# Kernel tuning notes

Hardware: AMD Instinct MI355X
Metric: run time of the kernel (lower is better)

The kernel has to match this reference:

```python
import jax, jax.numpy as jnp
import numpy as np

PAD_IDX = 1  # matches init_kwargs pad_idx
TLEN, BATCH, D_IN = 50, 16, 512
SRC_LEN, VOCAB, CVOCAB = 200, 20000, 20400


def setup_inputs() -> dict:
    key = jax.random.key(0)
    k1, k2, k3, k4, k5, k6, k7 = jax.random.split(key, 7)
    hidden = jax.random.normal(k1, (TLEN, BATCH, D_IN), dtype=jnp.float32)
    attn = jax.random.uniform(k2, (TLEN, BATCH, SRC_LEN), dtype=jnp.float32)
    # src_map is a sparse one-hot indicator: each source position maps to one extended-vocab id
    src_ids = jax.random.randint(k3, (SRC_LEN, BATCH), 0, CVOCAB)
    src_map = jax.nn.one_hot(src_ids, CVOCAB, dtype=jnp.float32)  # (src_len, batch, cvocab)
    s = 1.0 / np.sqrt(D_IN)
    W = jax.random.uniform(k4, (VOCAB, D_IN), dtype=jnp.float32, minval=-s, maxval=s)
    b = jax.random.uniform(k5, (VOCAB,), dtype=jnp.float32, minval=-s, maxval=s)
    Wc = jax.random.uniform(k6, (1, D_IN), dtype=jnp.float32, minval=-s, maxval=s)
    bc = jax.random.uniform(k7, (1,), dtype=jnp.float32, minval=-s, maxval=s)
    return {"hidden": hidden, "attn": attn, "src_map": src_map, "W": W, "b": b, "Wc": Wc, "bc": bc}


def reference(hidden, attn, src_map, W, b, Wc, bc):
    tlen, batch, _ = hidden.shape
    src_len, _, cvocab = src_map.shape
    logits = jnp.einsum('tbd,vd->tbv', hidden, W) + b            # (tlen, batch, vocab)
    # faithful to torch: logits[:, pad_idx] = -inf (indexes the batch dim!)
    logits = logits.at[:, PAD_IDX, :].set(-jnp.inf)
    prob = jax.nn.softmax(logits, axis=1)                        # softmax over dim 1, as in source
    p_copy = jax.nn.sigmoid(jnp.einsum('tbd,od->tbo', hidden, Wc) + bc)  # (tlen, batch, 1)
    out_prob = prob * (1.0 - p_copy)                             # (tlen, batch, vocab)
    mul_attn = attn * p_copy                                     # (tlen, batch, src_len)
    # bmm over batch with one-hot src_map: effectively a scatter-add into extended vocab
    copy_prob = jnp.einsum('tbs,sbv->tbv', mul_attn, src_map)    # (tlen, batch, cvocab)
    # faithful to the split/stack/transpose permutation in the source
    flat = copy_prob.reshape(tlen * batch, cvocab)
    copy_prob = flat.reshape(batch, tlen, cvocab).swapaxes(0, 1) # (tlen, batch, cvocab)
    copy_prob = copy_prob.at[:, :, :out_prob.shape[2]].add(out_prob)
    return copy_prob
```

## Files before the change

### kernel.cpp

```cpp
#include <hip/hip_runtime.h>
#include <cstdint>
#include <cstddef>

#define TLEN    50
#define BATCH   16
#define D_IN    512
#define SRC_LEN 200
#define VOCAB   20000
#define CVOCAB  20400

typedef __bf16 bf16x8 __attribute__((ext_vector_type(8)));
typedef float  f32x4  __attribute__((ext_vector_type(4)));

#define GEMM_BLOCKS 157
#define ZERO_BLOCKS 40
#define SCAN_BLOCKS (SRC_LEN * BATCH)
#define NTHREADS 256

__global__ __launch_bounds__(NTHREADS, 2)
void fused_main(const float* __restrict__ hidden,
                const float* __restrict__ src_map,
                const float* __restrict__ W,
                const float* __restrict__ Wc,
                const float* __restrict__ bc,
                float* __restrict__ out,
                int* __restrict__ src_ids)
{
    const int bid = blockIdx.x;
    const int tid = threadIdx.x;

    if (bid < GEMM_BLOCKS) {
        __shared__ __align__(16) __bf16 Alds[BATCH][D_IN + 8];
        __shared__ float WcLds[D_IN];
        __shared__ float pcLds[BATCH];

        for (int i = tid; i < D_IN; i += NTHREADS) WcLds[i] = Wc[i];
        const float bc0 = bc[0];

        const int lane = tid & 63;
        const int wv   = tid >> 6;
        const int l15  = lane & 15;
        const int q    = lane >> 4;
        const int colbase = bid * 128 + wv * 32;

        bf16x8 bfrag[2][16];
        bool act[2];
        {
            bf16x8 zf;
            #pragma unroll
            for (int j = 0; j < 8; ++j) zf[j] = (__bf16)0.0f;
            #pragma unroll
            for (int g = 0; g < 2; ++g) {
                const int vb = colbase + g * 16;
                act[g] = (vb < VOCAB);
                #pragma unroll
                for (int c = 0; c < 16; ++c) bfrag[g][c] = zf;
                if (act[g]) {
                    const float* wrow = W + (size_t)(vb + l15) * D_IN + q * 8;
                    #pragma unroll
                    for (int c = 0; c < 16; ++c) {
                        float4 f0 = *(const float4*)(wrow + c * 32);
                        float4 f1 = *(const float4*)(wrow + c * 32 + 4);
                        bf16x8 bf;
                        bf[0] = (__bf16)f0.x; bf[1] = (__bf16)f0.y;
                        bf[2] = (__bf16)f0.z; bf[3] = (__bf16)f0.w;
                        bf[4] = (__bf16)f1.x; bf[5] = (__bf16)f1.y;
                        bf[6] = (__bf16)f1.z; bf[7] = (__bf16)f1.w;
                        bfrag[g][c] = bf;
                    }
                }
            }
        }

        for (int t = 0; t < TLEN; ++t) {
            __syncthreads();
            #pragma unroll
            for (int i = 0; i < 8; ++i) {
                const int f = tid + i * NTHREADS;
                const int b = f >> 7;
                const int k = (f & 127) * 4;
                float4 v4 = *(const float4*)(hidden + (size_t)(t * BATCH + b) * D_IN + k);
                __bf16* dst = &Alds[b][k];
                dst[0] = (__bf16)v4.x; dst[1] = (__bf16)v4.y;
                dst[2] = (__bf16)v4.z; dst[3] = (__bf16)v4.w;
            }
            __syncthreads();

            {
                const int b = tid >> 4, l = tid & 15;
                float s = 0.f;
                #pragma unroll
                for (int j = 0; j < 32; ++j) {
                    const int k = l + j * 16;
                    s += (float)Alds[b][k] * WcLds[k];
                }
                #pragma unroll
                for (int o = 1; o < 16; o <<= 1) s += __shfl_xor(s, o, 16);
                if (l == 0) pcLds[b] = 1.0f / (1.0f + __expf(-(s + bc0)));
            }

            f32x4 acc0 = {0.f, 0.f, 0.f, 0.f};
            f32x4 acc1 = {0.f, 0.f, 0.f, 0.f};
            const __bf16* arow = &Alds[l15][q * 8];
            #pragma unroll
            for (int c = 0; c < 16; ++c) {
                bf16x8 af = *(const bf16x8*)(arow + c * 32);
                acc0 = __builtin_amdgcn_mfma_f32_16x16x32_bf16(af, bfrag[0][c], acc0, 0, 0, 0);
                acc1 = __builtin_amdgcn_mfma_f32_16x16x32_bf16(af, bfrag[1][c], acc1, 0, 0, 0);
            }
            __syncthreads();

            #pragma unroll
            for (int g = 0; g < 2; ++g) {
                f32x4 acc = g ? acc1 : acc0;
                float mx = -INFINITY;
                #pragma unroll
                for (int r = 0; r < 4; ++r) {
                    const int b = q * 4 + r;
                    if (b != 1) mx = fmaxf(mx, acc[r]);
                }
                mx = fmaxf(mx, __shfl_xor(mx, 16));
                mx = fmaxf(mx, __shfl_xor(mx, 32));
                float e[4], s = 0.f;
                #pragma unroll
                for (int r = 0; r < 4; ++r) {
                    const int b = q * 4 + r;
                    e[r] = (b == 1) ? 0.f : __expf(acc[r] - mx);
                    s += e[r];
                }
                s += __shfl_xor(s, 16);
                s += __shfl_xor(s, 32);
                const float inv = 1.0f / s;
                if (act[g]) {
                    const int v = colbase + g * 16 + l15;
                    #pragma unroll
                    for (int r = 0; r < 4; ++r) {
                        const int b = q * 4 + r;
                        out[(size_t)(t * BATCH + b) * CVOCAB + v] =
                            e[r] * inv * (1.0f - pcLds[b]);
                    }
                }
            }
        }
    } else if (bid < GEMM_BLOCKS + ZERO_BLOCKS) {
        const int zb = bid - GEMM_BLOCKS;
        const float4 z = {0.f, 0.f, 0.f, 0.f};
        for (int i = tid; i < 2000; i += NTHREADS) {
            const int f = zb * 2000 + i;
            const int r = f / 100;
            const int c = f % 100;
            *(float4*)(out + (size_t)r * CVOCAB + VOCAB + c * 4) = z;
        }
    } else {
        const int row = bid - GEMM_BLOCKS - ZERO_BLOCKS;
        const float4* base = (const float4*)(src_map + (size_t)row * CVOCAB);
        int found = -1;
        for (int i0 = tid; i0 < 1275; i0 += NTHREADS) {
            float4 x0 = base[i0];
            float4 x1 = base[i0 + 1275];
            float4 x2 = base[i0 + 2550];
            float4 x3 = base[i0 + 3825];
            #pragma unroll
            for (int seg = 0; seg < 4; ++seg) {
                float4 x = seg == 0 ? x0 : seg == 1 ? x1 : seg == 2 ? x2 : x3;
                const int e0 = (i0 + seg * 1275) * 4;
                if (x.x > 0.5f) found = e0;
                if (x.y > 0.5f) found = e0 + 1;
                if (x.z > 0.5f) found = e0 + 2;
                if (x.w > 0.5f) found = e0 + 3;
            }
        }
        if (found >= 0) src_ids[row] = found;
    }
}

__global__ __launch_bounds__(64)
void scatter_copy(const float* __restrict__ hidden,
                  const float* __restrict__ attn,
                  const float* __restrict__ Wc,
                  const float* __restrict__ bc,
                  const int* __restrict__ src_ids,
                  float* __restrict__ out)
{
    const int p = blockIdx.x;
    const int b = p & 15;
    const int l = threadIdx.x;

    float s = 0.f;
    const float* hrow = hidden + (size_t)p * D_IN;
    #pragma unroll
    for (int j = 0; j < 8; ++j) s += hrow[l + 64 * j] * Wc[l + 64 * j];
    #pragma unroll
    for (int o = 1; o < 64; o <<= 1) s += __shfl_xor(s, o);
    const float pc = 1.0f / (1.0f + __expf(-(s + bc[0])));

    const int b2 = p / 50;
    const int t2 = p % 50;
    const size_t obase = (size_t)(t2 * BATCH + b2) * CVOCAB;
    const float* arow = attn + (size_t)p * SRC_LEN;
    for (int si = l; si < SRC_LEN; si += 64) {
        const int id = src_ids[si * BATCH + b];
        const float val = arow[si] * pc;
        if ((unsigned)id < (unsigned)CVOCAB)
            atomicAdd(out + obase + id, val);
    }
}

extern "C" void kernel_launch(void* const* d_in, const int* in_sizes, int n_in,
                              void* d_out, int out_size, void* d_ws, size_t ws_size,
                              hipStream_t stream)
{
    const float* hidden  = (const float*)d_in[0];
    const float* attn    = (const float*)d_in[1];
    const float* src_map = (const float*)d_in[2];
    const float* W       = (const float*)d_in[3];
    const float* Wc      = (const float*)d_in[5];
    const float* bc      = (const float*)d_in[6];
    float* out   = (float*)d_out;
    int* src_ids = (int*)d_ws;

    fused_main<<<dim3(GEMM_BLOCKS + ZERO_BLOCKS + SCAN_BLOCKS), dim3(NTHREADS), 0, stream>>>(
        hidden, src_map, W, Wc, bc, out, src_ids);
    scatter_copy<<<dim3(TLEN * BATCH), dim3(64), 0, stream>>>(
        hidden, attn, Wc, bc, src_ids, out);
}
```

Baseline: 516.3 us.

## Split GEMM over time chunks, precompute p_copy in a separate kernel

A small pre-kernel now computes the p_copy gate once per (t,b) row into workspace, replacing the per-block recomputation inside the GEMM loop and inside the scatter kernel. The GEMM blocks are doubled by splitting the time dimension in two, so each column tile handles half the timesteps. The A operand is read directly from global memory into registers and converted to bf16, which removes the LDS staging and block-wide barriers. The cost is a third kernel launch, W fragments loaded and converted twice, and uncoalesced hidden reads that rely on the cache.

```diff
diff --git a/kernel.cpp b/kernel.cpp
--- a/kernel.cpp
+++ b/kernel.cpp
@@ -12,17 +12,39 @@
 typedef __bf16 bf16x8 __attribute__((ext_vector_type(8)));
 typedef float  f32x4  __attribute__((ext_vector_type(4)));
 
-#define GEMM_BLOCKS 157
+#define TSPLIT  2
+#define TCHUNK  (TLEN / TSPLIT)
+#define COLTILES 157
+#define GEMM_BLOCKS (COLTILES * TSPLIT)
 #define ZERO_BLOCKS 40
 #define SCAN_BLOCKS (SRC_LEN * BATCH)
 #define NTHREADS 256
+
+__global__ __launch_bounds__(256)
+void pc_kernel(const float* __restrict__ hidden,
+               const float* __restrict__ Wc,
+               const float* __restrict__ bc,
+               float* __restrict__ pc)
+{
+    const int row  = blockIdx.x * 4 + (threadIdx.x >> 6);
+    const int lane = threadIdx.x & 63;
+    const float* h = hidden + (size_t)row * D_IN + lane * 8;
+    float4 h0 = *(const float4*)(h);
+    float4 h1 = *(const float4*)(h + 4);
+    float4 w0 = *(const float4*)(Wc + lane * 8);
+    float4 w1 = *(const float4*)(Wc + lane * 8 + 4);
+    float s = h0.x*w0.x + h0.y*w0.y + h0.z*w0.z + h0.w*w0.w
+            + h1.x*w1.x + h1.y*w1.y + h1.z*w1.z + h1.w*w1.w;
+    #pragma unroll
+    for (int o = 1; o < 64; o <<= 1) s += __shfl_xor(s, o);
+    if (lane == 0) pc[row] = 1.0f / (1.0f + __expf(-(s + bc[0])));
+}
 
 __global__ __launch_bounds__(NTHREADS, 2)
 void fused_main(const float* __restrict__ hidden,
                 const float* __restrict__ src_map,
                 const float* __restrict__ W,
-                const float* __restrict__ Wc,
-                const float* __restrict__ bc,
+                const float* __restrict__ pc,
                 float* __restrict__ out,
                 int* __restrict__ src_ids)
 {
@@ -30,18 +52,15 @@
     const int tid = threadIdx.x;
 
     if (bid < GEMM_BLOCKS) {
-        __shared__ __align__(16) __bf16 Alds[BATCH][D_IN + 8];
-        __shared__ float WcLds[D_IN];
-        __shared__ float pcLds[BATCH];
-
-        for (int i = tid; i < D_IN; i += NTHREADS) WcLds[i] = Wc[i];
-        const float bc0 = bc[0];
+        const int ct = bid / TSPLIT;
+        const int th = bid % TSPLIT;
+        const int t0 = th * TCHUNK;
 
         const int lane = tid & 63;
         const int wv   = tid >> 6;
         const int l15  = lane & 15;
         const int q    = lane >> 4;
-        const int colbase = bid * 128 + wv * 32;
+        const int colbase = ct * 128 + wv * 32;
 
         bf16x8 bfrag[2][16];
         bool act[2];
@@ -72,60 +91,37 @@
             }
         }
 
-        for (int t = 0; t < TLEN; ++t) {
-            __syncthreads();
-            #pragma unroll
-            for (int i = 0; i < 8; ++i) {
-                const int f = tid + i * NTHREADS;
-                const int b = f >> 7;
-                const int k = (f & 127) * 4;
-                float4 v4 = *(const float4*)(hidden + (size_t)(t * BATCH + b) * D_IN + k);
-                __bf16* dst = &Alds[b][k];
-                dst[0] = (__bf16)v4.x; dst[1] = (__bf16)v4.y;
-                dst[2] = (__bf16)v4.z; dst[3] = (__bf16)v4.w;
-            }
-            __syncthreads();
-
-            {
-                const int b = tid >> 4, l = tid & 15;
-                float s = 0.f;
-                #pragma unroll
-                for (int j = 0; j < 32; ++j) {
-                    const int k = l + j * 16;
-                    s += (float)Alds[b][k] * WcLds[k];
-                }
-                #pragma unroll
-                for (int o = 1; o < 16; o <<= 1) s += __shfl_xor(s, o, 16);
-                if (l == 0) pcLds[b] = 1.0f / (1.0f + __expf(-(s + bc0)));
-            }
-
+        for (int t = t0; t < t0 + TCHUNK; ++t) {
+            const float* hbase = hidden + ((size_t)t * BATCH + l15) * D_IN + q * 8;
             f32x4 acc0 = {0.f, 0.f, 0.f, 0.f};
             f32x4 acc1 = {0.f, 0.f, 0.f, 0.f};
-            const __bf16* arow = &Alds[l15][q * 8];
             #pragma unroll
             for (int c = 0; c < 16; ++c) {
-                bf16x8 af = *(const bf16x8*)(arow + c * 32);
+                float4 f0 = *(const float4*)(hbase + c * 32);
+                float4 f1 = *(const float4*)(hbase + c * 32 + 4);
+                bf16x8 af;
+                af[0] = (__bf16)f0.x; af[1] = (__bf16)f0.y;
+                af[2] = (__bf16)f0.z; af[3] = (__bf16)f0.w;
+                af[4] = (__bf16)f1.x; af[5] = (__bf16)f1.y;
+                af[6] = (__bf16)f1.z; af[7] = (__bf16)f1.w;
                 acc0 = __builtin_amdgcn_mfma_f32_16x16x32_bf16(af, bfrag[0][c], acc0, 0, 0, 0);
                 acc1 = __builtin_amdgcn_mfma_f32_16x16x32_bf16(af, bfrag[1][c], acc1, 0, 0, 0);
             }
-            __syncthreads();
+            float4 pc4 = *(const float4*)(pc + t * 16 + q * 4);
 
             #pragma unroll
             for (int g = 0; g < 2; ++g) {
                 f32x4 acc = g ? acc1 : acc0;
                 float mx = -INFINITY;
                 #pragma unroll
-                for (int r = 0; r < 4; ++r) {
-                    const int b = q * 4 + r;
-                    if (b != 1) mx = fmaxf(mx, acc[r]);
-                }
+                for (int r = 0; r < 4; ++r)
+                    if (q * 4 + r != 1) mx = fmaxf(mx, acc[r]);
                 mx = fmaxf(mx, __shfl_xor(mx, 16));
                 mx = fmaxf(mx, __shfl_xor(mx, 32));
                 float e[4], s = 0.f;
                 #pragma unroll
                 for (int r = 0; r < 4; ++r) {
-                    const int b = q * 4 + r;
-                    e[r] = (b == 1) ? 0.f : __expf(acc[r] - mx);
+                    e[r] = (q * 4 + r == 1) ? 0.f : __expf(acc[r] - mx);
                     s += e[r];
                 }
                 s += __shfl_xor(s, 16);
@@ -137,7 +133,7 @@
                     for (int r = 0; r < 4; ++r) {
                         const int b = q * 4 + r;
                         out[(size_t)(t * BATCH + b) * CVOCAB + v] =
-                            e[r] * inv * (1.0f - pcLds[b]);
+                            e[r] * inv * (1.0f - pc4[r]);
                     }
                 }
             }
@@ -174,36 +170,21 @@
     }
 }
 
-__global__ __launch_bounds__(64)
-void scatter_copy(const float* __restrict__ hidden,
-                  const float* __restrict__ attn,
-                  const float* __restrict__ Wc,
-                  const float* __restrict__ bc,
+__global__ __launch_bounds__(256)
+void scatter_copy(const float* __restrict__ attn,
+                  const float* __restrict__ pc,
                   const int* __restrict__ src_ids,
                   float* __restrict__ out)
 {
-    const int p = blockIdx.x;
-    const int b = p & 15;
-    const int l = threadIdx.x;
-
-    float s = 0.f;
-    const float* hrow = hidden + (size_t)p * D_IN;
-    #pragma unroll
-    for (int j = 0; j < 8; ++j) s += hrow[l + 64 * j] * Wc[l + 64 * j];
-    #pragma unroll
-    for (int o = 1; o < 64; o <<= 1) s += __shfl_xor(s, o);
-    const float pc = 1.0f / (1.0f + __expf(-(s + bc[0])));
-
-    const int b2 = p / 50;
-    const int t2 = p % 50;
-    const size_t obase = (size_t)(t2 * BATCH + b2) * CVOCAB;
-    const float* arow = attn + (size_t)p * SRC_LEN;
-    for (int si = l; si < SRC_LEN; si += 64) {
-        const int id = src_ids[si * BATCH + b];
-        const float val = arow[si] * pc;
-        if ((unsigned)id < (unsigned)CVOCAB)
-            atomicAdd(out + obase + id, val);
-    }
+    const int p  = blockIdx.x;
+    const int si = threadIdx.x;
+    if (si >= SRC_LEN) return;
+    const int b  = p & 15;
+    const size_t obase = (size_t)((p % TLEN) * BATCH + (p / TLEN)) * CVOCAB;
+    const int id = src_ids[si * BATCH + b];
+    const float val = attn[(size_t)p * SRC_LEN + si] * pc[p];
+    if ((unsigned)id < (unsigned)CVOCAB)
+        atomicAdd(out + obase + id, val);
 }
 
 extern "C" void kernel_launch(void* const* d_in, const int* in_sizes, int n_in,
@@ -218,9 +199,10 @@
     const float* bc      = (const float*)d_in[6];
     float* out   = (float*)d_out;
     int* src_ids = (int*)d_ws;
-
+    float* pc    = (float*)d_ws + 3200;
+
+    pc_kernel<<<dim3(200), dim3(256), 0, stream>>>(hidden, Wc, bc, pc);
     fused_main<<<dim3(GEMM_BLOCKS + ZERO_BLOCKS + SCAN_BLOCKS), dim3(NTHREADS), 0, stream>>>(
-        hidden, src_map, W, Wc, bc, out, src_ids);
-    scatter_copy<<<dim3(TLEN * BATCH), dim3(64), 0, stream>>>(
-        hidden, attn, Wc, bc, src_ids, out);
-}
+        hidden, src_map, W, pc, out, src_ids);
+    scatter_copy<<<dim3(TLEN * BATCH), dim3(256), 0, stream>>>(attn, pc, src_ids, out);
+}
```

Result: slower. 599.3 us (+16.1%).
